# Performance work log

Measured on AMD Instinct MI355X. Metric: run time of the kernel, lower is better.

## Reference

```python
import jax, jax.numpy as jnp
import numpy as np

NUM_HEADS = 16
HEAD_DIM = 96          # dim=1536 / 16 heads
ROPE_HALF = HEAD_DIM // 2   # 48 rotary frequencies
FREQ_PER_AXIS = ROPE_HALF // 3  # 16 frequencies per 3D coordinate axis
ROPE_BASE = 10000.0


def _rope_sincos(coords):
    # coords: [B, T, 3] -> sin, cos: [B, T, ROPE_HALF]
    inv_freq = 1.0 / (ROPE_BASE ** (jnp.arange(FREQ_PER_AXIS, dtype=jnp.float32) / FREQ_PER_AXIS))
    # angles per axis: [B, T, 3, F] -> concat axes -> [B, T, 3*F]
    ang = coords[..., :, None] * inv_freq  # [B, T, 3, F]
    ang = ang.reshape(*coords.shape[:-1], ROPE_HALF)
    return jnp.sin(ang), jnp.cos(ang)


def _apply_rotary(x, sin, cos):
    # x: [B, H, T, D]; sin/cos: [B, T, D/2] broadcast over heads
    s = sin[:, None, :, :]
    c = cos[:, None, :, :]
    x1, x2 = x[..., :ROPE_HALF], x[..., ROPE_HALF:]
    return jnp.concatenate([x1 * c - x2 * s, x2 * c + x1 * s], axis=-1)


def setup_inputs() -> dict:
    key = jax.random.key(0)
    ks = jax.random.split(key, 8)
    B, Tq, Tk, D = 2, 1024, 2048, 1536
    std = 1.0 / np.sqrt(D)
    return {
        "x": jax.random.normal(ks[0], (B, Tq, D), jnp.float32),
        "memory": jax.random.normal(ks[1], (B, Tk, D), jnp.float32),
        "query_coords": jax.random.normal(ks[2], (B, Tq, 3), jnp.float32),
        "memory_coords": jax.random.normal(ks[3], (B, Tk, 3), jnp.float32),
        "Wq": jax.random.normal(ks[4], (D, D), jnp.float32) * std,
        "bq": jnp.zeros((D,), jnp.float32),
        "Wk": jax.random.normal(ks[5], (D, D), jnp.float32) * std,
        "bk": jnp.zeros((D,), jnp.float32),
        "Wv": jax.random.normal(ks[6], (D, D), jnp.float32) * std,
        "bv": jnp.zeros((D,), jnp.float32),
        "Wo": jax.random.normal(ks[7], (D, D), jnp.float32) * std,
        "bo": jnp.zeros((D,), jnp.float32),
    }


def reference(x, memory, query_coords, memory_coords, Wq, bq, Wk, bk, Wv, bv, Wo, bo):
    B, Tq, D = x.shape
    Tk = memory.shape[1]
    H, Hd = NUM_HEADS, HEAD_DIM

    # projections (nn.Linear: y = x @ W^T + b)
    q = (jnp.einsum('btd,ed->bte', x, Wq) + bq).reshape(B, Tq, H, Hd).transpose(0, 2, 1, 3)
    k = (jnp.einsum('btd,ed->bte', memory, Wk) + bk).reshape(B, Tk, H, Hd).transpose(0, 2, 1, 3)
    v = (jnp.einsum('btd,ed->bte', memory, Wv) + bv).reshape(B, Tk, H, Hd).transpose(0, 2, 1, 3)

    # 3D-coordinate RoPE (identity augmentation: shift=0, jitter=1, rescale=1)
    q_sin, q_cos = _rope_sincos(query_coords)
    k_sin, k_cos = _rope_sincos(memory_coords)
    q = _apply_rotary(q, q_sin, q_cos)
    k = _apply_rotary(k, k_sin, k_cos)

    # SDPA (standard scaling): softmax(q k^T / sqrt(Hd)) v
    scale = 1.0 / jnp.sqrt(jnp.asarray(Hd, jnp.float32))
    scores = jnp.einsum('bhqd,bhkd->bhqk', q, k) * scale
    attn = jax.nn.softmax(scores, axis=-1)
    out = jnp.einsum('bhqk,bhkd->bhqd', attn, v)  # [B, H, Tq, Hd]

    out = out.transpose(0, 2, 1, 3).reshape(B, Tq, D)
    return jnp.einsum('btd,ed->bte', out, Wo) + bo
```

## Files before the change

kernel.cpp:

```cpp
#include <hip/hip_runtime.h>
#include <math.h>

typedef _Float16 f16;
typedef __attribute__((ext_vector_type(4))) _Float16 f16x4;
typedef __attribute__((ext_vector_type(8))) _Float16 f16x8;
typedef __attribute__((ext_vector_type(4))) float f32x4;
typedef __attribute__((ext_vector_type(16))) float f32x16;

#define NB 2
#define NH 16
#define TQ 1024
#define TK 2048
#define DM 1536
#define HD 96
#define RH 48

__device__ __forceinline__ f32x4 mfma16(f16x8 a, f16x8 b, f32x4 c) {
    return __builtin_amdgcn_mfma_f32_16x16x32_f16(a, b, c, 0, 0, 0);
}

#define GLDS16(gptr, lptr) __builtin_amdgcn_global_load_lds( \
    (const __attribute__((address_space(1))) unsigned int*)(gptr), \
    (__attribute__((address_space(3))) unsigned int*)(lptr), 16, 0, 0)

__global__ void cvt_w4(const float4* __restrict__ W0, const float4* __restrict__ W1,
                       const float4* __restrict__ W2, const float4* __restrict__ W3,
                       f16x4* __restrict__ o0, f16x4* __restrict__ o1,
                       f16x4* __restrict__ o2, f16x4* __restrict__ o3, int n4) {
    int i = blockIdx.x * 256 + threadIdx.x;
    if (i >= n4) return;
    const float4* in = blockIdx.y == 0 ? W0 : blockIdx.y == 1 ? W1 : blockIdx.y == 2 ? W2 : W3;
    f16x4* out      = blockIdx.y == 0 ? o0 : blockIdx.y == 1 ? o1 : blockIdx.y == 2 ? o2 : o3;
    float4 v = in[i];
    f16x4 o;
    o[0] = (f16)v.x; o[1] = (f16)v.y; o[2] = (f16)v.z; o[3] = (f16)v.w;
    out[i] = o;
}

__global__ void cvt_xm(const float4* __restrict__ X, const float4* __restrict__ M,
                       f16x4* __restrict__ ox, f16x4* __restrict__ om, int nx4, int nm4) {
    int i = blockIdx.x * 256 + threadIdx.x;
    int n = blockIdx.y == 0 ? nx4 : nm4;
    if (i >= n) return;
    const float4* in = blockIdx.y == 0 ? X : M;
    f16x4* out = blockIdx.y == 0 ? ox : om;
    float4 v = in[i];
    f16x4 o;
    o[0] = (f16)v.x; o[1] = (f16)v.y; o[2] = (f16)v.z; o[3] = (f16)v.w;
    out[i] = o;
}

__global__ void rope_tab2(const float* __restrict__ cq, const float* __restrict__ cm,
                          float* __restrict__ sq, float* __restrict__ cqo,
                          float* __restrict__ sk, float* __restrict__ cko,
                          int nq, int nk) {
    int i = blockIdx.x * 256 + threadIdx.x;
    int n = blockIdx.y == 0 ? nq : nk;
    if (i >= n) return;
    const float* coords = blockIdx.y == 0 ? cq : cm;
    float* sinT = blockIdx.y == 0 ? sq : sk;
    float* cosT = blockIdx.y == 0 ? cqo : cko;
    int bt = i / 48, idx = i - bt * 48;
    int axis = idx >> 4, f = idx & 15;
    float inv = powf(10000.f, -(float)f * (1.f / 16.f));
    float ang = coords[bt * 3 + axis] * inv;
    sinT[i] = sinf(ang);
    cosT[i] = cosf(ang);
}

__global__ void rope_apply_k(f16* __restrict__ qk, const float* __restrict__ sinT,
                             const float* __restrict__ cosT, int T, int stride,
                             float scale, int n) {
    int i = blockIdx.x * 256 + threadIdx.x;
    if (i >= n) return;
    int p = i % 48;
    int rest = i / 48;
    int t = rest % T;
    int b = rest / (NH * T);
    long base = (long)rest * stride;
    float x1 = (float)qk[base + p];
    float x2 = (float)qk[base + p + RH];
    int ti = (b * T + t) * 48 + p;
    float s = sinT[ti], c = cosT[ti];
    qk[base + p]      = (f16)((x1 * c - x2 * s) * scale);
    qk[base + p + RH] = (f16)((x2 * c + x1 * s) * scale);
}

template <int MODE, int BM>
__global__ __launch_bounds__(512, 2) void gemm3p(
    const f16* __restrict__ A, const f16* __restrict__ Wa, const f16* __restrict__ Wb,
    const float* __restrict__ ba, const float* __restrict__ bb,
    void* __restrict__ outa, void* __restrict__ outb,
    int M, int N, int K, int T) {
    constexpr int RA = BM / 64;
    constexpr int RB = 2;
    constexpr int LPS = RA + RB;
    constexpr int NW_M = BM / 64;
    constexpr int NI = (NW_M == 4) ? 4 : 2;
    constexpr int BUF = (BM + 128) * 64;

    __shared__ f16 Buf[3][BUF];

    const int tid = threadIdx.x;
    const int w = tid >> 6, lane = tid & 63;
    const int l15 = lane & 15, g = lane >> 4;
    int bx = blockIdx.x;
    const f16* W = Wa; const float* bias = ba; void* outp = outa;
    bool sel = false;
    if (MODE == 4 && bx >= 12) { sel = true; W = Wb; bias = bb; outp = outb; bx -= 12; }
    const int m0 = blockIdx.y * BM, n0 = bx * 128;
    const int wm = (w % NW_M) * 64;
    const int wn = (w / NW_M) * (NI * 16);

    int asrc[RA], bsrc[RB];
#pragma unroll
    for (int r = 0; r < RA; r++) {
        int L = r * 8192 + w * 1024 + lane * 16;
        int row = L >> 7, seg = (L >> 4) & 7;
        asrc[r] = row * K + ((seg ^ (row & 7)) << 3);
    }
#pragma unroll
    for (int r = 0; r < RB; r++) {
        int L = r * 8192 + w * 1024 + lane * 16;
        int row = L >> 7, seg = (L >> 4) & 7;
        bsrc[r] = row * K + ((seg ^ (row & 7)) << 3);
    }
    const f16* Ag = A + (long)m0 * K;
    const f16* Bg = W + (long)n0 * K;

#define STAGE3(bufi, kt) do { \
    _Pragma("unroll") for (int r_ = 0; r_ < RA; r_++) \
        GLDS16(Ag + asrc[r_] + (kt) * 64, &Buf[bufi][r_ * 4096 + w * 512]); \
    _Pragma("unroll") for (int r_ = 0; r_ < RB; r_++) \
        GLDS16(Bg + bsrc[r_] + (kt) * 64, &Buf[bufi][BM * 64 + r_ * 4096 + w * 512]); \
} while (0)

    f32x4 acc[4][NI] = {};
    const int NT = K >> 6;

    STAGE3(0, 0);
    STAGE3(1, 1);

    int cur = 0;
    for (int t = 0; t < NT; ++t) {
        if constexpr (LPS == 6) asm volatile("s_waitcnt vmcnt(6)" ::: "memory");
        else                    asm volatile("s_waitcnt vmcnt(4)" ::: "memory");
        __builtin_amdgcn_s_barrier();
        __builtin_amdgcn_sched_barrier(0);

        if (t + 2 < NT) {
            int nb = cur + 2; if (nb >= 3) nb -= 3;
            STAGE3(nb, t + 2);
        }
        __builtin_amdgcn_sched_barrier(0);

        const f16* ab = &Buf[cur][0];
        const f16* bbp = &Buf[cur][BM * 64];
        f16x8 af[4][2], bf[NI][2];
#pragma unroll
        for (int i = 0; i < 4; i++)
#pragma unroll
            for (int s = 0; s < 2; s++) {
                int row = wm + i * 16 + l15, seg = s * 4 + g;
                af[i][s] = *(const f16x8*)&ab[row * 64 + ((seg ^ (row & 7)) << 3)];
            }
#pragma unroll
        for (int j = 0; j < NI; j++)
#pragma unroll
            for (int s = 0; s < 2; s++) {
                int row = wn + j * 16 + l15, seg = s * 4 + g;
                bf[j][s] = *(const f16x8*)&bbp[row * 64 + ((seg ^ (row & 7)) << 3)];
            }
        __builtin_amdgcn_s_setprio(1);
#pragma unroll
        for (int s = 0; s < 2; s++)
#pragma unroll
            for (int i = 0; i < 4; i++)
#pragma unroll
                for (int j = 0; j < NI; j++)
                    acc[i][j] = mfma16(af[i][s], bf[j][s], acc[i][j]);
        __builtin_amdgcn_s_setprio(0);

        cur += 1; if (cur >= 3) cur -= 3;
    }
#undef STAGE3

#pragma unroll
    for (int i = 0; i < 4; i++) {
#pragma unroll
        for (int j = 0; j < NI; j++) {
            const int n = n0 + wn + j * 16 + l15;
            const int mb = m0 + wm + i * 16 + g * 4;
            if (MODE == 4 && sel) {
                int bq = mb / T, t = mb - bq * T;
                int hh = n / HD, hd = n - hh * HD;
                f16x4 pk;
#pragma unroll
                for (int r = 0; r < 4; r++) pk[r] = (f16)(acc[i][j][r] + bias[n]);
                *(f16x4*)&((f16*)outp)[(((long)bq * NH + hh) * HD + hd) * TK + t] = pk;
            } else if (MODE == 4) {
#pragma unroll
                for (int r = 0; r < 4; r++) {
                    int m = mb + r;
                    int bq = m / T, t = m - bq * T;
                    int hh = n / HD, hd = n - hh * HD;
                    ((f16*)outp)[(((long)bq * NH + hh) * T + t) * 128 + hd] = (f16)(acc[i][j][r] + bias[n]);
                }
            } else if (MODE == 5) {
#pragma unroll
                for (int r = 0; r < 4; r++) {
                    int m = mb + r;
                    int bq = m / T, t = m - bq * T;
                    int hh = n / HD, hd = n - hh * HD;
                    ((f16*)outp)[(((long)bq * NH + hh) * T + t) * 96 + hd] = (f16)(acc[i][j][r] + bias[n]);
                }
            } else {
#pragma unroll
                for (int r = 0; r < 4; r++)
                    ((float*)outp)[(long)(mb + r) * N + n] = acc[i][j][r] + bias[n];
            }
        }
    }
}

__global__ __launch_bounds__(256, 2) void attn_fwd(
    const f16* __restrict__ Q, const f16* __restrict__ Kg,
    const f16* __restrict__ Vg, f16* __restrict__ O) {
    __shared__ f16 Kl[2][64 * 128];
    __shared__ f16 Vl[2][96 * 64];
    __shared__ f16 Pl[4][32 * 64];

    const int tid = threadIdx.x, w = tid >> 6, lane = tid & 63;
    const int q31 = lane & 31, hf = lane >> 5;
    const int half = w >> 1, u = w & 1;

    const int linear = blockIdx.x + (int)(gridDim.x * (blockIdx.y + gridDim.y * blockIdx.z));
    const int wid = (linear & 7) * 64 + (linear >> 3);
    const int qc = wid & 15, h = (wid >> 4) & 15, b = wid >> 8;

    const long kbase = (long)(b * NH + h) * TK * 128;
    const long vbase = (long)(b * NH + h) * HD * TK;
    const long qbase = (long)(b * NH + h) * TQ * 96;
    const int q0 = qc * 64 + u * 32;

    int ksrc[8], vsrc[6];
#pragma unroll
    for (int i = 0; i < 8; i++) {
        int L = (u * 8 + i) * 1024 + lane * 16;
        int r = L >> 8, s = (L >> 4) & 15;
        ksrc[i] = r * 128 + ((s ^ (r & 7)) << 3);
    }
#pragma unroll
    for (int i = 0; i < 6; i++) {
        int L = (u * 6 + i) * 1024 + lane * 16;
        int r = L >> 7, s = (L >> 4) & 7;
        vsrc[i] = r * TK + ((s ^ (r & 7)) << 3);
    }

    f16x8 qf[6];
#pragma unroll
    for (int s = 0; s < 6; s++)
        qf[s] = *(const f16x8*)&Q[qbase + (long)(q0 + q31) * 96 + hf * 8 + 16 * s];

    float mx = -3e38f, ls = 0.f;
    f32x16 acc[3] = {};

#define STAGE(c_) do { \
    const f16* kp_ = Kg + kbase + (long)(half * 16 + (c_)) * (64 * 128); \
    _Pragma("unroll") for (int i_ = 0; i_ < 8; i_++) \
        GLDS16(kp_ + ksrc[i_], &Kl[half][(u * 8 + i_) * 512]); \
    const f16* vp_ = Vg + vbase + (half * 16 + (c_)) * 64; \
    _Pragma("unroll") for (int i_ = 0; i_ < 6; i_++) \
        GLDS16(vp_ + vsrc[i_], &Vl[half][(u * 6 + i_) * 512]); \
} while (0)

    STAGE(0);

    for (int c = 0; c < 16; ++c) {
        __syncthreads();

        f32x16 st[2] = {};
#pragma unroll
        for (int kt = 0; kt < 2; kt++)
#pragma unroll
            for (int s = 0; s < 6; s++) {
                f16x8 kf = *(const f16x8*)&Kl[half][(kt * 32 + q31) * 128 +
                                                    (((hf + 2 * s) ^ (q31 & 7)) << 3)];
                st[kt] = __builtin_amdgcn_mfma_f32_32x32x16_f16(kf, qf[s], st[kt], 0, 0, 0);
            }

        float t16[16];
#pragma unroll
        for (int r = 0; r < 16; r++) t16[r] = fmaxf(st[0][r], st[1][r]);
#pragma unroll
        for (int o = 8; o >= 1; o >>= 1)
#pragma unroll
            for (int r = 0; r < o; r++) t16[r] = fmaxf(t16[r], t16[r + o]);
        float cm = fmaxf(t16[0], __shfl_xor(t16[0], 32));
        float mn = fmaxf(mx, cm);
        float corr = exp2f(mx - mn);
        mx = mn;
#pragma unroll
        for (int kt = 0; kt < 2; kt++)
#pragma unroll
            for (int r = 0; r < 16; r++) st[kt][r] = exp2f(st[kt][r] - mn);
        float s16[16];
#pragma unroll
        for (int r = 0; r < 16; r++) s16[r] = st[0][r] + st[1][r];
#pragma unroll
        for (int o = 8; o >= 1; o >>= 1)
#pragma unroll
            for (int r = 0; r < o; r++) s16[r] += s16[r + o];
        ls = ls * corr + s16[0];
#pragma unroll
        for (int dt = 0; dt < 3; dt++)
#pragma unroll
            for (int r = 0; r < 16; r++) acc[dt][r] *= corr;

#pragma unroll
        for (int kt = 0; kt < 2; kt++)
#pragma unroll
            for (int jq = 0; jq < 4; jq++) {
                f16x4 pk;
#pragma unroll
                for (int e = 0; e < 4; e++) pk[e] = (f16)st[kt][jq * 4 + e];
                int seg = kt * 4 + jq;
                *(f16x4*)&Pl[w][q31 * 64 + ((seg ^ (q31 & 7)) << 3) + hf * 4] = pk;
            }

#pragma unroll
        for (int ks = 0; ks < 4; ks++) {
            f16x8 pf = *(const f16x8*)&Pl[w][q31 * 64 + (((hf + 2 * ks) ^ (q31 & 7)) << 3)];
#pragma unroll
            for (int dt = 0; dt < 3; dt++) {
                f16x8 vf = *(const f16x8*)&Vl[half][(dt * 32 + q31) * 64 +
                                                    (((hf + 2 * ks) ^ (q31 & 7)) << 3)];
                acc[dt] = __builtin_amdgcn_mfma_f32_32x32x16_f16(vf, pf, acc[dt], 0, 0, 0);
            }
        }

        __syncthreads();
        if (c < 15) STAGE(c + 1);
    }

    ls += __shfl_xor(ls, 32);
    float* dump = (float*)&Kl[0][0] + u * (64 * 52);
    __syncthreads();
    if (half == 1) {
        float* dl = dump + lane * 52;
        dl[0] = mx; dl[1] = ls;
#pragma unroll
        for (int dt = 0; dt < 3; dt++)
#pragma unroll
            for (int r = 0; r < 16; r++) dl[2 + dt * 16 + r] = acc[dt][r];
    }
    __syncthreads();
    if (half == 0) {
        const float* dl = dump + lane * 52;
        float mb = dl[0], lsb = dl[1];
        float mf = fmaxf(mx, mb);
        float ca = exp2f(mx - mf), cb = exp2f(mb - mf);
        float inv = 1.f / (ls * ca + lsb * cb);
        const long orow = (long)(b * TQ + q0 + q31) * DM + h * 96;
#pragma unroll
        for (int dt = 0; dt < 3; dt++)
#pragma unroll
            for (int jq = 0; jq < 4; jq++) {
                f16x4 ov;
#pragma unroll
                for (int e = 0; e < 4; e++) {
                    int r = jq * 4 + e;
                    ov[e] = (f16)((acc[dt][r] * ca + dl[2 + dt * 16 + r] * cb) * inv);
                }
                *(f16x4*)&O[orow + dt * 32 + jq * 8 + hf * 4] = ov;
            }
    }
}

extern "C" void kernel_launch(void* const* d_in, const int* in_sizes, int n_in,
                              void* d_out, int out_size, void* d_ws, size_t ws_size,
                              hipStream_t stream) {
    const float* x   = (const float*)d_in[0];
    const float* mem = (const float*)d_in[1];
    const float* qc  = (const float*)d_in[2];
    const float* mc  = (const float*)d_in[3];
    const float* Wq  = (const float*)d_in[4];
    const float* bq  = (const float*)d_in[5];
    const float* Wk  = (const float*)d_in[6];
    const float* bk  = (const float*)d_in[7];
    const float* Wv  = (const float*)d_in[8];
    const float* bv  = (const float*)d_in[9];
    const float* Wo  = (const float*)d_in[10];
    const float* bo  = (const float*)d_in[11];
    float* out = (float*)d_out;

    const long nx  = (long)NB * TQ * DM;
    const long nm  = (long)NB * TK * DM;
    const long nw  = (long)DM * DM;
    const long nq  = (long)NB * NH * TQ * 96;
    const long nkp = (long)NB * NH * TK * 128;
    const long nvt = (long)NB * NH * HD * TK;

    char* ws = (char*)d_ws;
    size_t off = 0;
    auto alloc = [&](size_t bytes) { size_t o = off; off = (off + bytes + 255) & ~(size_t)255; return o; };
    f16* x16   = (f16*)(ws + alloc(nx * 2));
    f16* mem16 = (f16*)(ws + alloc(nm * 2));
    f16* wq16  = (f16*)(ws + alloc(nw * 2));
    f16* wk16  = (f16*)(ws + alloc(nw * 2));
    f16* wv16  = (f16*)(ws + alloc(nw * 2));
    f16* wo16  = (f16*)(ws + alloc(nw * 2));
    f16* q16   = (f16*)(ws + alloc(nq * 2));
    f16* k16p  = (f16*)(ws + alloc(nkp * 2));
    f16* vt16  = (f16*)(ws + alloc(nvt * 2));
    float* sinq = (float*)(ws + alloc((size_t)NB * TQ * 48 * 4));
    float* cosq = (float*)(ws + alloc((size_t)NB * TQ * 48 * 4));
    float* sink = (float*)(ws + alloc((size_t)NB * TK * 48 * 4));
    float* cosk = (float*)(ws + alloc((size_t)NB * TK * 48 * 4));
    f16* at16 = x16;

    cvt_w4<<<dim3((int)(nw / 4 / 256), 4), 256, 0, stream>>>(
        (const float4*)Wq, (const float4*)Wk, (const float4*)Wv, (const float4*)Wo,
        (f16x4*)wq16, (f16x4*)wk16, (f16x4*)wv16, (f16x4*)wo16, (int)(nw / 4));
    cvt_xm<<<dim3((int)(nm / 4 / 256), 2), 256, 0, stream>>>(
        (const float4*)x, (const float4*)mem, (f16x4*)x16, (f16x4*)mem16,
        (int)(nx / 4), (int)(nm / 4));

    rope_tab2<<<dim3((NB * TK * 48 + 255) / 256, 2), 256, 0, stream>>>(
        qc, mc, sinq, cosq, sink, cosk, NB * TQ * 48, NB * TK * 48);

    gemm3p<5, 128><<<dim3(12, 16), 512, 0, stream>>>(
        x16, wq16, nullptr, bq, nullptr, q16, nullptr, NB * TQ, DM, DM, TQ);
    gemm3p<4, 256><<<dim3(24, 16), 512, 0, stream>>>(
        mem16, wk16, wv16, bk, bv, k16p, vt16, NB * TK, DM, DM, TK);

    const float qscale = 0.10206207261596577f * 1.4426950408889634f;
    rope_apply_k<<<(NB * NH * TQ * 48 + 255) / 256, 256, 0, stream>>>(
        q16, sinq, cosq, TQ, 96, qscale, NB * NH * TQ * 48);
    rope_apply_k<<<(NB * NH * TK * 48 + 255) / 256, 256, 0, stream>>>(
        k16p, sink, cosk, TK, 128, 1.0f, NB * NH * TK * 48);

    attn_fwd<<<dim3(16, 16, 2), 256, 0, stream>>>(q16, k16p, vt16, at16);

    gemm3p<1, 128><<<dim3(12, 16), 512, 0, stream>>>(
        at16, wo16, nullptr, bo, nullptr, out, nullptr, NB * TQ, DM, DM, TQ);
}
```

Measured before the change: 184.8 us.

## Retile GEMMs to K=32 stages with 64x64 warp tiles and fewer threads

```diff
diff --git a/kernel.cpp b/kernel.cpp
--- a/kernel.cpp
+++ b/kernel.cpp
@@ -87,19 +87,20 @@
 }
 
 template <int MODE, int BM>
-__global__ __launch_bounds__(512, 2) void gemm3p(
+__global__ __launch_bounds__(BM == 256 ? 512 : 256, BM == 256 ? 4 : 3) void gemm3p(
     const f16* __restrict__ A, const f16* __restrict__ Wa, const f16* __restrict__ Wb,
     const float* __restrict__ ba, const float* __restrict__ bb,
     void* __restrict__ outa, void* __restrict__ outb,
     int M, int N, int K, int T) {
-    constexpr int RA = BM / 64;
-    constexpr int RB = 2;
+    constexpr int TPB = (BM == 256) ? 512 : 256;
+    constexpr int NW_M = (BM == 256) ? 4 : 2;
+    constexpr int RA = (BM * 64) / (TPB * 16);
+    constexpr int RB = (128 * 64) / (TPB * 16);
     constexpr int LPS = RA + RB;
-    constexpr int NW_M = BM / 64;
-    constexpr int NI = (NW_M == 4) ? 4 : 2;
-    constexpr int BUF = (BM + 128) * 64;
-
-    __shared__ f16 Buf[3][BUF];
+    constexpr int ABUF = BM * 32;
+    constexpr int BUFSZ = (BM + 128) * 32;
+
+    __shared__ f16 Buf[3][BUFSZ];
 
     const int tid = threadIdx.x;
     const int w = tid >> 6, lane = tid & 63;
@@ -110,85 +111,82 @@
     if (MODE == 4 && bx >= 12) { sel = true; W = Wb; bias = bb; outp = outb; bx -= 12; }
     const int m0 = blockIdx.y * BM, n0 = bx * 128;
     const int wm = (w % NW_M) * 64;
-    const int wn = (w / NW_M) * (NI * 16);
+    const int wn = (w / NW_M) * 64;
 
     int asrc[RA], bsrc[RB];
 #pragma unroll
     for (int r = 0; r < RA; r++) {
-        int L = r * 8192 + w * 1024 + lane * 16;
-        int row = L >> 7, seg = (L >> 4) & 7;
-        asrc[r] = row * K + ((seg ^ (row & 7)) << 3);
+        int L = r * (TPB * 16) + tid * 16;
+        int row = L >> 6, seg = (L >> 4) & 3;
+        asrc[r] = row * K + ((seg ^ ((row ^ (row >> 2)) & 3)) << 3);
     }
 #pragma unroll
     for (int r = 0; r < RB; r++) {
-        int L = r * 8192 + w * 1024 + lane * 16;
-        int row = L >> 7, seg = (L >> 4) & 7;
-        bsrc[r] = row * K + ((seg ^ (row & 7)) << 3);
+        int L = r * (TPB * 16) + tid * 16;
+        int row = L >> 6, seg = (L >> 4) & 3;
+        bsrc[r] = row * K + ((seg ^ ((row ^ (row >> 2)) & 3)) << 3);
     }
     const f16* Ag = A + (long)m0 * K;
     const f16* Bg = W + (long)n0 * K;
 
+    int aoff[4], boff[4];
+#pragma unroll
+    for (int i = 0; i < 4; i++) {
+        int row = wm + i * 16 + l15;
+        aoff[i] = row * 32 + ((g ^ ((row ^ (row >> 2)) & 3)) << 3);
+    }
+#pragma unroll
+    for (int j = 0; j < 4; j++) {
+        int row = wn + j * 16 + l15;
+        boff[j] = ABUF + row * 32 + ((g ^ ((row ^ (row >> 2)) & 3)) << 3);
+    }
+
 #define STAGE3(bufi, kt) do { \
     _Pragma("unroll") for (int r_ = 0; r_ < RA; r_++) \
-        GLDS16(Ag + asrc[r_] + (kt) * 64, &Buf[bufi][r_ * 4096 + w * 512]); \
+        GLDS16(Ag + asrc[r_] + (kt) * 32, &Buf[bufi][r_ * (TPB * 8) + w * 512]); \
     _Pragma("unroll") for (int r_ = 0; r_ < RB; r_++) \
-        GLDS16(Bg + bsrc[r_] + (kt) * 64, &Buf[bufi][BM * 64 + r_ * 4096 + w * 512]); \
+        GLDS16(Bg + bsrc[r_] + (kt) * 32, &Buf[bufi][ABUF + r_ * (TPB * 8) + w * 512]); \
 } while (0)
 
-    f32x4 acc[4][NI] = {};
-    const int NT = K >> 6;
+    f32x4 acc[4][4] = {};
+    const int NT = K >> 5;
 
     STAGE3(0, 0);
     STAGE3(1, 1);
 
-    int cur = 0;
-    for (int t = 0; t < NT; ++t) {
-        if constexpr (LPS == 6) asm volatile("s_waitcnt vmcnt(6)" ::: "memory");
-        else                    asm volatile("s_waitcnt vmcnt(4)" ::: "memory");
-        __builtin_amdgcn_s_barrier();
-        __builtin_amdgcn_sched_barrier(0);
-
-        if (t + 2 < NT) {
-            int nb = cur + 2; if (nb >= 3) nb -= 3;
-            STAGE3(nb, t + 2);
+#pragma unroll 1
+    for (int t = 0; t < NT; t += 3) {
+#pragma unroll
+        for (int u = 0; u < 3; u++) {
+            asm volatile("s_waitcnt vmcnt(%0)" :: "n"(LPS) : "memory");
+            __builtin_amdgcn_s_barrier();
+            __builtin_amdgcn_sched_barrier(0);
+            if (t + u + 2 < NT) {
+                constexpr int NB3[3] = {2, 0, 1};
+                STAGE3(NB3[u], t + u + 2);
+            }
+            __builtin_amdgcn_sched_barrier(0);
+
+            f16x8 af[4], bf[4];
+#pragma unroll
+            for (int i = 0; i < 4; i++) af[i] = *(const f16x8*)&Buf[u][aoff[i]];
+#pragma unroll
+            for (int j = 0; j < 4; j++) bf[j] = *(const f16x8*)&Buf[u][boff[j]];
+            __builtin_amdgcn_s_setprio(1);
+#pragma unroll
+            for (int i = 0; i < 4; i++)
+#pragma unroll
+                for (int j = 0; j < 4; j++)
+                    acc[i][j] = mfma16(af[i], bf[j], acc[i][j]);
+            __builtin_amdgcn_s_setprio(0);
         }
-        __builtin_amdgcn_sched_barrier(0);
-
-        const f16* ab = &Buf[cur][0];
-        const f16* bbp = &Buf[cur][BM * 64];
-        f16x8 af[4][2], bf[NI][2];
-#pragma unroll
-        for (int i = 0; i < 4; i++)
-#pragma unroll
-            for (int s = 0; s < 2; s++) {
-                int row = wm + i * 16 + l15, seg = s * 4 + g;
-                af[i][s] = *(const f16x8*)&ab[row * 64 + ((seg ^ (row & 7)) << 3)];
-            }
-#pragma unroll
-        for (int j = 0; j < NI; j++)
-#pragma unroll
-            for (int s = 0; s < 2; s++) {
-                int row = wn + j * 16 + l15, seg = s * 4 + g;
-                bf[j][s] = *(const f16x8*)&bbp[row * 64 + ((seg ^ (row & 7)) << 3)];
-            }
-        __builtin_amdgcn_s_setprio(1);
-#pragma unroll
-        for (int s = 0; s < 2; s++)
-#pragma unroll
-            for (int i = 0; i < 4; i++)
-#pragma unroll
-                for (int j = 0; j < NI; j++)
-                    acc[i][j] = mfma16(af[i][s], bf[j][s], acc[i][j]);
-        __builtin_amdgcn_s_setprio(0);
-
-        cur += 1; if (cur >= 3) cur -= 3;
     }
 #undef STAGE3
 
 #pragma unroll
     for (int i = 0; i < 4; i++) {
 #pragma unroll
-        for (int j = 0; j < NI; j++) {
+        for (int j = 0; j < 4; j++) {
             const int n = n0 + wn + j * 16 + l15;
             const int mb = m0 + wm + i * 16 + g * 4;
             if (MODE == 4 && sel) {
@@ -429,7 +427,7 @@
     rope_tab2<<<dim3((NB * TK * 48 + 255) / 256, 2), 256, 0, stream>>>(
         qc, mc, sinq, cosq, sink, cosk, NB * TQ * 48, NB * TK * 48);
 
-    gemm3p<5, 128><<<dim3(12, 16), 512, 0, stream>>>(
+    gemm3p<5, 128><<<dim3(12, 16), 256, 0, stream>>>(
         x16, wq16, nullptr, bq, nullptr, q16, nullptr, NB * TQ, DM, DM, TQ);
     gemm3p<4, 256><<<dim3(24, 16), 512, 0, stream>>>(
         mem16, wk16, wv16, bk, bv, k16p, vt16, NB * TK, DM, DM, TK);
@@ -442,6 +440,6 @@
 
     attn_fwd<<<dim3(16, 16, 2), 256, 0, stream>>>(q16, k16p, vt16, at16);
 
-    gemm3p<1, 128><<<dim3(12, 16), 512, 0, stream>>>(
+    gemm3p<1, 128><<<dim3(12, 16), 256, 0, stream>>>(
         at16, wo16, nullptr, bo, nullptr, out, nullptr, NB * TQ, DM, DM, TQ);
 }
```

Measured after the change: 205.4 us, median of 2. 11.1% more time.
